# Kernel optimization log

Measured on AMD Instinct MI355X. Metric: run time of the kernel, lower is better.

The kernel has to match this reference:

```python
import jax, jax.numpy as jnp
import numpy as np

INPUT_DIM = 1024
K_DIM = 1024
V_DIM = 1024
HEAD = 16
N = 4096


def setup_inputs() -> dict:
    key = jax.random.key(0)
    ks = jax.random.split(key, 6)
    # kaiming_uniform_(a=1): bound = sqrt(6 / ((1+1)*fan_in)) = sqrt(3/fan_in)
    def ku(k, shape):
        fan_in = shape[1]
        b = np.sqrt(3.0 / fan_in)
        return jax.random.uniform(k, shape, jnp.float32, -b, b)
    x = jax.random.normal(ks[0], (1, N, INPUT_DIM), jnp.float32)
    Wq = ku(ks[1], (K_DIM, INPUT_DIM))
    Wk = ku(ks[2], (K_DIM, INPUT_DIM))
    Wv = ku(ks[3], (V_DIM, INPUT_DIM))
    Wo = ku(ks[4], (V_DIM, V_DIM))
    bo = jnp.zeros((V_DIM,), jnp.float32)
    return {"x": x, "Wq": Wq, "Wk": Wk, "Wv": Wv, "Wo": Wo, "bo": bo}


def reference(x, Wq, Wk, Wv, Wo, bo):
    # x: [1, N, C]
    n = x.shape[1]
    hd_k = K_DIM // HEAD
    hd_v = V_DIM // HEAD
    q = jnp.einsum('bnc,kc->bnk', x, Wq).reshape(1, n, HEAD, hd_k).transpose(0, 2, 1, 3)
    k = jnp.einsum('bnc,kc->bnk', x, Wk).reshape(1, n, HEAD, hd_k).transpose(0, 2, 1, 3)
    v = jnp.einsum('bnc,kc->bnk', x, Wv).reshape(1, n, HEAD, hd_v).transpose(0, 2, 1, 3)
    scale = 1.0 / np.sqrt(hd_k).astype(np.float32)
    scores = jnp.einsum('bhqd,bhkd->bhqk', q, k) * scale  # [1,H,N,N]
    attn = jax.nn.softmax(scores, axis=-1)
    ctx = jnp.einsum('bhqk,bhkd->bhqd', attn, v)  # [1,H,N,hd_v]
    ctx = ctx.transpose(0, 2, 1, 3).reshape(1, n, V_DIM)
    out = jnp.einsum('bnv,ov->bno', ctx, Wo) + bo
    return out
```

## Files before the change

### kernel.cpp

```cpp
#include <hip/hip_runtime.h>

typedef short bf16x8 __attribute__((ext_vector_type(8)));
typedef float f32x4 __attribute__((ext_vector_type(4)));
typedef float f32x16 __attribute__((ext_vector_type(16)));
typedef unsigned short u16;
typedef unsigned short u16x8 __attribute__((ext_vector_type(8)));
typedef unsigned int u32;
typedef unsigned int u32x2 __attribute__((ext_vector_type(2)));
typedef unsigned int u32x4 __attribute__((ext_vector_type(4)));

#define MFMA16(a, b, c) __builtin_amdgcn_mfma_f32_16x16x32_bf16((a), (b), (c), 0, 0, 0)
#define MFMA32(a, b, c) __builtin_amdgcn_mfma_f32_32x32x16_bf16((a), (b), (c), 0, 0, 0)

__device__ __forceinline__ u16 f2bf(float f) {
  unsigned u = __builtin_bit_cast(unsigned, f);
  return (u16)((u + 0x7fffu + ((u >> 16) & 1u)) >> 16);
}

__device__ __forceinline__ unsigned cvt_pk_bf16(float lo, float hi) {
  unsigned r;
  asm("v_cvt_pk_bf16_f32 %0, %1, %2" : "=v"(r) : "v"(lo), "v"(hi));
  return r;
}

__device__ __forceinline__ void gload_lds16(const u16* g, u16* lds) {
  __builtin_amdgcn_global_load_lds((__attribute__((address_space(1))) void*)g,
                                   (__attribute__((address_space(3))) void*)lds,
                                   16, 0, 0);
}

__device__ __forceinline__ void publish_barrier() {
  asm volatile("s_waitcnt lgkmcnt(0)" ::: "memory");
  __builtin_amdgcn_sched_barrier(0);
  __builtin_amdgcn_s_barrier();
}

__global__ __launch_bounds__(256) void cvt_all(
    const float* __restrict__ x, const float* __restrict__ w0,
    const float* __restrict__ w1, const float* __restrict__ w2,
    const float* __restrict__ w3, u16* __restrict__ xb, u16* __restrict__ wb) {
  long i = (long)(blockIdx.x * 256 + threadIdx.x) * 8;
  const float* src; u16* dst; long off;
  if (i < 4194304) { src = x; dst = xb; off = i; }
  else {
    long k = i - 4194304; int w = (int)(k >> 20); off = k & 1048575;
    src = (w == 0) ? w0 : (w == 1) ? w1 : (w == 2) ? w2 : w3;
    dst = wb + (long)w * 1048576;
  }
  float4 a = *(const float4*)(src + off);
  float4 b = *(const float4*)(src + off + 4);
  u16x8 o;
  o[0] = f2bf(a.x); o[1] = f2bf(a.y); o[2] = f2bf(a.z); o[3] = f2bf(a.w);
  o[4] = f2bf(b.x); o[5] = f2bf(b.y); o[6] = f2bf(b.z); o[7] = f2bf(b.w);
  *(u16x8*)(dst + off) = o;
}

template <int MODE>
__global__ __launch_bounds__(256) void gemm_bt(
    const u16* __restrict__ A, const u16* __restrict__ Bw,
    u16* __restrict__ Co, float* __restrict__ Cf, const float* __restrict__ bias) {
  constexpr int K = 1024;
  __shared__ u16 As[128 * 32];
  __shared__ u16 Bs[128 * 32];
  const int tid = threadIdx.x, w = tid >> 6, l = tid & 63;
  const int lg = l >> 4, lr = l & 15;
  const int mb = blockIdx.x;
  int mat, nb;
  if (MODE == 0) { mat = blockIdx.y >> 3; nb = blockIdx.y & 7; }
  else           { mat = 0;               nb = blockIdx.y;     }
  const u16* __restrict__ Bp = Bw + (long)mat * 1048576;
  const int wr = w >> 1, wc = w & 1;
  f32x4 acc[4][4] = {};
  const int srow = (l >> 2), scol = (l & 3) * 8;
  for (int kt = 0; kt < K / 32; ++kt) {
    const int kb = kt * 32;
    __syncthreads();
#pragma unroll
    for (int i = 0; i < 2; ++i) {
      int r = w * 32 + i * 16 + srow;
      gload_lds16(A  + (long)(mb * 128 + r) * K + kb + scol, &As[(w * 2 + i) * 512]);
      gload_lds16(Bp + (long)(nb * 128 + r) * K + kb + scol, &Bs[(w * 2 + i) * 512]);
    }
    __syncthreads();
    bf16x8 af[4], bf[4];
#pragma unroll
    for (int m = 0; m < 4; ++m) af[m] = *(const bf16x8*)&As[(wr * 64 + m * 16 + lr) * 32 + lg * 8];
#pragma unroll
    for (int n = 0; n < 4; ++n) bf[n] = *(const bf16x8*)&Bs[(wc * 64 + n * 16 + lr) * 32 + lg * 8];
#pragma unroll
    for (int m = 0; m < 4; ++m)
#pragma unroll
      for (int n = 0; n < 4; ++n)
        acc[m][n] = MFMA16(af[m], bf[n], acc[m][n]);
  }
  const int row0 = mb * 128 + wr * 64, col0 = nb * 128 + wc * 64;
#pragma unroll
  for (int m = 0; m < 4; ++m)
#pragma unroll
    for (int n = 0; n < 4; ++n)
#pragma unroll
      for (int rr = 0; rr < 4; ++rr) {
        int row = row0 + m * 16 + lg * 4 + rr;
        int col = col0 + n * 16 + lr;
        float v = acc[m][n][rr];
        if (MODE == 0) {
          if (mat == 0) v *= 0.18033688011112042f;
          Co[(long)mat * 4194304 + (long)row * 1024 + col] = f2bf(v);
        } else {
          Cf[(long)row * 1024 + col] = v + bias[col];
        }
      }
}

__global__ __launch_bounds__(256) void attn(
    const u16* __restrict__ Qg, const u16* __restrict__ Kg,
    const u16* __restrict__ Vg, u16* __restrict__ Og) {
  __shared__ u16 Ksb[2 * 4096];
  __shared__ u16 Vsb[2 * 64 * 72];
  const int tid = threadIdx.x, w = tid >> 6, l = tid & 63;
  const int l31 = l & 31, hi = l >> 5;

  const int lin = blockIdx.x;
  const int xcd = lin & 7, idx = lin >> 3;
  const int head = xcd * 2 + (idx >> 5), qt = idx & 31;
  const int hb = head * 64;
  const int q0 = qt * 128 + w * 32;

  const u16* __restrict__ Kh = Kg + hb;

  bf16x8 qf[4];
#pragma unroll
  for (int st = 0; st < 4; ++st)
    qf[st] = *(const bf16x8*)&Qg[(long)(q0 + l31) * 1024 + hb + st * 16 + hi * 8];

  f32x16 o0 = {}, o1 = {};
  f32x4 lsv = {};

  const int kr = tid >> 3, c8 = tid & 7;
  const u16* Vgp = Vg + hb + c8 * 8;
  bf16x8 va0, va1;

  const int krow = tid >> 3;
  const int ksrc = (((tid & 7) * 16) ^ ((krow & 7) << 4)) >> 1;
  u16* kdst = Ksb + w * 512;

#define KSTAGE(t_, db_)                                                       \
  {                                                                           \
    gload_lds16(Kh + (long)((t_) * 64 + krow) * 1024 + ksrc,                  \
                kdst + (db_) * 4096);                                         \
    gload_lds16(Kh + (long)((t_) * 64 + 32 + krow) * 1024 + ksrc,             \
                kdst + (db_) * 4096 + 2048);                                  \
  }

#define VLOAD(t_)                                                     \
  {                                                                   \
    long r0_ = (long)(t_) * 64 + kr * 2;                              \
    va0 = *(const bf16x8*)&Vgp[r0_ * 1024];                           \
    va1 = *(const bf16x8*)&Vgp[(r0_ + 1) * 1024];                     \
  }

#define VWRITE(db_)                                                       \
  {                                                                       \
    const int cw = (kr ^ (c8 << 2)) * 2;                                  \
    u16* d_ = Vsb + (db_) * 4608;                                         \
    u32x4 A_ = __builtin_bit_cast(u32x4, va0);                            \
    u32x4 B_ = __builtin_bit_cast(u32x4, va1);                            \
    _Pragma("unroll") for (int dd = 0; dd < 4; ++dd) {                    \
      u32 pe = __builtin_amdgcn_perm(B_[dd], A_[dd], 0x05040100u);        \
      u32 po = __builtin_amdgcn_perm(B_[dd], A_[dd], 0x07060302u);        \
      *(u32*)&d_[(c8 * 8 + 2 * dd) * 72 + cw] = pe;                       \
      *(u32*)&d_[(c8 * 8 + 2 * dd + 1) * 72 + cw] = po;                   \
    }                                                                     \
  }

#define KFRAG(kf_, db_)                                                       \
  {                                                                           \
    _Pragma("unroll") for (int tt = 0; tt < 2; ++tt)                          \
      _Pragma("unroll") for (int st = 0; st < 4; ++st) {                      \
        const int row_ = tt * 32 + l31;                                       \
        const int boff_ = (st * 32 + hi * 16) ^ ((row_ & 7) << 4);            \
        (kf_)[tt][st] =                                                       \
            *(const bf16x8*)&Ksb[(db_) * 4096 + row_ * 64 + (boff_ >> 1)];    \
      }                                                                       \
  }

#define QKT(S0_, S1_, db_)                                                    \
  {                                                                           \
    bf16x8 kf_[2][4];                                                         \
    KFRAG(kf_, db_);                                                          \
    S0_ = (f32x16){};                                                         \
    S1_ = (f32x16){};                                                         \
    __builtin_amdgcn_s_setprio(1);                                            \
    _Pragma("unroll") for (int st = 0; st < 4; ++st) {                        \
      S0_ = MFMA32(kf_[0][st], qf[st], S0_);                                  \
      S1_ = MFMA32(kf_[1][st], qf[st], S1_);                                  \
    }                                                                         \
    __builtin_amdgcn_s_setprio(0);                                            \
  }

#define PACKCHUNK(SX, base_, pb_)                                             \
  {                                                                           \
    u32 a0_ = cvt_pk_bf16((SX)[(base_) + 0], (SX)[(base_) + 1]);              \
    u32 b0_ = cvt_pk_bf16((SX)[(base_) + 4], (SX)[(base_) + 5]);              \
    u32 a1_ = cvt_pk_bf16((SX)[(base_) + 2], (SX)[(base_) + 3]);              \
    u32 b1_ = cvt_pk_bf16((SX)[(base_) + 6], (SX)[(base_) + 7]);              \
    u32x2 r0_ = __builtin_amdgcn_permlane32_swap(a0_, b0_, false, false);     \
    u32x2 r1_ = __builtin_amdgcn_permlane32_swap(a1_, b1_, false, false);     \
    u32x4 fv_;                                                                \
    fv_[0] = r0_[0]; fv_[1] = r1_[0]; fv_[2] = r0_[1]; fv_[3] = r1_[1];       \
    (pb_) = __builtin_bit_cast(bf16x8, fv_);                                  \
  }

#define FINISH(SC0, SC1, db_)                                                 \
  {                                                                           \
    _Pragma("unroll") for (int r = 0; r < 16; ++r) {                          \
      SC0[r] = __builtin_amdgcn_exp2f(SC0[r]);                                \
      SC1[r] = __builtin_amdgcn_exp2f(SC1[r]);                                \
    }                                                                         \
    const u16* myV = Vsb + (db_) * 4608;                                      \
    _Pragma("unroll") for (int c = 0; c < 4; ++c) {                           \
      bf16x8 pb;                                                              \
      if (c < 2) { PACKCHUNK(SC0, (c & 1) * 8, pb); }                         \
      else       { PACKCHUNK(SC1, (c & 1) * 8, pb); }                         \
      const int sw0 = ((8 * c + 4 * hi) ^ (((l31 >> 3) & 7) << 2)) * 2;       \
      const int sw1 = ((8 * c + 4 * hi) ^ ((((l31 + 32) >> 3) & 7) << 2)) * 2;\
      bf16x8 vf0 = *(const bf16x8*)&myV[l31 * 72 + sw0];                      \
      bf16x8 vf1 = *(const bf16x8*)&myV[(32 + l31) * 72 + sw1];               \
      __builtin_amdgcn_s_setprio(1);                                          \
      o0 = MFMA32(vf0, pb, o0);                                               \
      o1 = MFMA32(vf1, pb, o1);                                               \
      __builtin_amdgcn_s_setprio(0);                                          \
    }                                                                         \
    _Pragma("unroll") for (int r2 = 0; r2 < 4; ++r2)                          \
      _Pragma("unroll") for (int j = 0; j < 4; ++j)                           \
        lsv[j] += SC0[r2 * 4 + j] + SC1[r2 * 4 + j];                          \
  }

  f32x16 Sa0, Sa1, Sb0, Sb1;

  KSTAGE(0, 0);
  VLOAD(0);
  asm volatile("s_waitcnt vmcnt(0)" ::: "memory");
  publish_barrier();
  QKT(Sa0, Sa1, 0);
  KSTAGE(1, 1);
  VWRITE(0);
  asm volatile("s_waitcnt vmcnt(0)" ::: "memory");
  publish_barrier();

#define BODY(t_, db_, SC0, SC1, SN0, SN1)                                     \
  {                                                                           \
    KSTAGE((t_) + 2, db_);                                                    \
    VLOAD((t_) + 1);                                                          \
    QKT(SN0, SN1, (db_) ^ 1);                                                 \
    FINISH(SC0, SC1, db_);                                                    \
    VWRITE((db_) ^ 1);                                                        \
    publish_barrier();                                                        \
  }

  for (int i = 0; i < 31; ++i) {
    BODY(2 * i, 0, Sa0, Sa1, Sb0, Sb1);
    BODY(2 * i + 1, 1, Sb0, Sb1, Sa0, Sa1);
  }
  {
    VLOAD(63);
    QKT(Sb0, Sb1, 1);
    FINISH(Sa0, Sa1, 0);
    VWRITE(1);
    publish_barrier();
  }
  FINISH(Sb0, Sb1, 1);

  {
    float sls = (lsv[0] + lsv[1]) + (lsv[2] + lsv[3]);
    float s = sls + __shfl_xor(sls, 32);
    float inv = 1.0f / s;
#pragma unroll
    for (int dt = 0; dt < 2; ++dt) {
#pragma unroll
      for (int r2 = 0; r2 < 4; ++r2) {
        float v0 = dt ? o1[r2 * 4 + 0] : o0[r2 * 4 + 0];
        float v1 = dt ? o1[r2 * 4 + 1] : o0[r2 * 4 + 1];
        float v2 = dt ? o1[r2 * 4 + 2] : o0[r2 * 4 + 2];
        float v3 = dt ? o1[r2 * 4 + 3] : o0[r2 * 4 + 3];
        uint2 pk;
        pk.x = cvt_pk_bf16(v0 * inv, v1 * inv);
        pk.y = cvt_pk_bf16(v2 * inv, v3 * inv);
        const int d0 = dt * 32 + 8 * r2 + 4 * hi;
        *(uint2*)&Og[(long)(q0 + l31) * 1024 + hb + d0] = pk;
      }
    }
  }
#undef KSTAGE
#undef VLOAD
#undef VWRITE
#undef KFRAG
#undef QKT
#undef PACKCHUNK
#undef FINISH
#undef BODY
}

extern "C" void kernel_launch(void* const* d_in, const int* in_sizes, int n_in,
                              void* d_out, int out_size, void* d_ws, size_t ws_size,
                              hipStream_t stream) {
  const float* x  = (const float*)d_in[0];
  const float* Wq = (const float*)d_in[1];
  const float* Wk = (const float*)d_in[2];
  const float* Wv = (const float*)d_in[3];
  const float* Wo = (const float*)d_in[4];
  const float* bo = (const float*)d_in[5];
  float* out = (float*)d_out;

  u16* xb  = (u16*)d_ws;
  u16* wb  = xb + 4194304;
  u16* qkv = wb + 4194304;
  u16* ctx = qkv + 3 * 4194304;

  cvt_all<<<dim3(4096), dim3(256), 0, stream>>>(x, Wq, Wk, Wv, Wo, xb, wb);
  gemm_bt<0><<<dim3(32, 24), dim3(256), 0, stream>>>(xb, wb, qkv, nullptr, nullptr);
  attn<<<dim3(512), dim3(256), 0, stream>>>(qkv, qkv + 4194304, qkv + 8388608, ctx);
  gemm_bt<1><<<dim3(32, 8), dim3(256), 0, stream>>>(ctx, wb + 3 * 1048576, nullptr, out, bo);
}
```

Baseline: 161.1 us.

## Process two KV tiles per barrier interval with quad-buffered K/V LDS

Restructures the attention main loop so each barrier interval stages and consumes two 64-key tiles, using four LDS buffers for K and V instead of two. Barrier count is halved and the next pair of tiles is prefetched while the current pair runs QK^T and PV. In exchange, LDS use doubles (to about 68KB per block), which may lower occupancy. The skewed pipeline that overlapped the next tile's QK^T with the current tile's softmax/PV is dropped, and more registers are live for the extra V loads and score tiles.

```diff
diff --git a/kernel.cpp b/kernel.cpp
--- a/kernel.cpp
+++ b/kernel.cpp
@@ -115,8 +115,8 @@
 __global__ __launch_bounds__(256) void attn(
     const u16* __restrict__ Qg, const u16* __restrict__ Kg,
     const u16* __restrict__ Vg, u16* __restrict__ Og) {
-  __shared__ u16 Ksb[2 * 4096];
-  __shared__ u16 Vsb[2 * 64 * 72];
+  __shared__ u16 Ksb[4 * 4096];
+  __shared__ u16 Vsb[4 * 4608];
   const int tid = threadIdx.x, w = tid >> 6, l = tid & 63;
   const int l31 = l & 31, hi = l >> 5;
 
@@ -138,39 +138,52 @@
 
   const int kr = tid >> 3, c8 = tid & 7;
   const u16* Vgp = Vg + hb + c8 * 8;
-  bf16x8 va0, va1;
+  bf16x8 va0, va1, vb0, vb1;
 
   const int krow = tid >> 3;
   const int ksrc = (((tid & 7) * 16) ^ ((krow & 7) << 4)) >> 1;
   u16* kdst = Ksb + w * 512;
 
-#define KSTAGE(t_, db_)                                                       \
+#define KSTAGE2(t_, b0_, b1_)                                                 \
   {                                                                           \
     gload_lds16(Kh + (long)((t_) * 64 + krow) * 1024 + ksrc,                  \
-                kdst + (db_) * 4096);                                         \
+                kdst + (b0_) * 4096);                                         \
     gload_lds16(Kh + (long)((t_) * 64 + 32 + krow) * 1024 + ksrc,             \
-                kdst + (db_) * 4096 + 2048);                                  \
-  }
-
-#define VLOAD(t_)                                                     \
+                kdst + (b0_) * 4096 + 2048);                                  \
+    gload_lds16(Kh + (long)((t_) * 64 + 64 + krow) * 1024 + ksrc,             \
+                kdst + (b1_) * 4096);                                         \
+    gload_lds16(Kh + (long)((t_) * 64 + 96 + krow) * 1024 + ksrc,             \
+                kdst + (b1_) * 4096 + 2048);                                  \
+  }
+
+#define VLOAD2(t_)                                                    \
   {                                                                   \
     long r0_ = (long)(t_) * 64 + kr * 2;                              \
     va0 = *(const bf16x8*)&Vgp[r0_ * 1024];                           \
     va1 = *(const bf16x8*)&Vgp[(r0_ + 1) * 1024];                     \
-  }
-
-#define VWRITE(db_)                                                       \
-  {                                                                       \
-    const int cw = (kr ^ (c8 << 2)) * 2;                                  \
-    u16* d_ = Vsb + (db_) * 4608;                                         \
-    u32x4 A_ = __builtin_bit_cast(u32x4, va0);                            \
-    u32x4 B_ = __builtin_bit_cast(u32x4, va1);                            \
-    _Pragma("unroll") for (int dd = 0; dd < 4; ++dd) {                    \
-      u32 pe = __builtin_amdgcn_perm(B_[dd], A_[dd], 0x05040100u);        \
-      u32 po = __builtin_amdgcn_perm(B_[dd], A_[dd], 0x07060302u);        \
-      *(u32*)&d_[(c8 * 8 + 2 * dd) * 72 + cw] = pe;                       \
-      *(u32*)&d_[(c8 * 8 + 2 * dd + 1) * 72 + cw] = po;                   \
-    }                                                                     \
+    vb0 = *(const bf16x8*)&Vgp[(r0_ + 64) * 1024];                    \
+    vb1 = *(const bf16x8*)&Vgp[(r0_ + 65) * 1024];                    \
+  }
+
+#define VWRITE2(b0_, b1_)                                                  \
+  {                                                                        \
+    const int cw = (kr ^ (c8 << 2)) * 2;                                   \
+    u16* da_ = Vsb + (b0_) * 4608;                                         \
+    u16* db_ = Vsb + (b1_) * 4608;                                         \
+    u32x4 A_ = __builtin_bit_cast(u32x4, va0);                             \
+    u32x4 B_ = __builtin_bit_cast(u32x4, va1);                             \
+    u32x4 C_ = __builtin_bit_cast(u32x4, vb0);                             \
+    u32x4 D_ = __builtin_bit_cast(u32x4, vb1);                             \
+    _Pragma("unroll") for (int dd = 0; dd < 4; ++dd) {                     \
+      u32 pe = __builtin_amdgcn_perm(B_[dd], A_[dd], 0x05040100u);         \
+      u32 po = __builtin_amdgcn_perm(B_[dd], A_[dd], 0x07060302u);         \
+      u32 qe = __builtin_amdgcn_perm(D_[dd], C_[dd], 0x05040100u);         \
+      u32 qo = __builtin_amdgcn_perm(D_[dd], C_[dd], 0x07060302u);         \
+      *(u32*)&da_[(c8 * 8 + 2 * dd) * 72 + cw] = pe;                       \
+      *(u32*)&da_[(c8 * 8 + 2 * dd + 1) * 72 + cw] = po;                   \
+      *(u32*)&db_[(c8 * 8 + 2 * dd) * 72 + cw] = qe;                       \
+      *(u32*)&db_[(c8 * 8 + 2 * dd + 1) * 72 + cw] = qo;                   \
+    }                                                                      \
   }
 
 #define KFRAG(kf_, db_)                                                       \
@@ -236,40 +249,33 @@
         lsv[j] += SC0[r2 * 4 + j] + SC1[r2 * 4 + j];                          \
   }
 
-  f32x16 Sa0, Sa1, Sb0, Sb1;
-
-  KSTAGE(0, 0);
-  VLOAD(0);
+#define INTERVAL(i_, p_, stage_)                                              \
+  {                                                                           \
+    if (stage_) {                                                             \
+      KSTAGE2(2 * (i_) + 2, (p_) ^ 2, ((p_) ^ 2) + 1);                        \
+      VLOAD2(2 * (i_) + 2);                                                   \
+    }                                                                         \
+    f32x16 Sa0, Sa1, Sb0, Sb1;                                                \
+    QKT(Sa0, Sa1, p_);                                                        \
+    QKT(Sb0, Sb1, (p_) + 1);                                                  \
+    FINISH(Sa0, Sa1, p_);                                                     \
+    FINISH(Sb0, Sb1, (p_) + 1);                                               \
+    if (stage_) VWRITE2((p_) ^ 2, ((p_) ^ 2) + 1);                            \
+    publish_barrier();                                                        \
+  }
+
+  KSTAGE2(0, 0, 1);
+  VLOAD2(0);
+  VWRITE2(0, 1);
   asm volatile("s_waitcnt vmcnt(0)" ::: "memory");
   publish_barrier();
-  QKT(Sa0, Sa1, 0);
-  KSTAGE(1, 1);
-  VWRITE(0);
-  asm volatile("s_waitcnt vmcnt(0)" ::: "memory");
-  publish_barrier();
-
-#define BODY(t_, db_, SC0, SC1, SN0, SN1)                                     \
-  {                                                                           \
-    KSTAGE((t_) + 2, db_);                                                    \
-    VLOAD((t_) + 1);                                                          \
-    QKT(SN0, SN1, (db_) ^ 1);                                                 \
-    FINISH(SC0, SC1, db_);                                                    \
-    VWRITE((db_) ^ 1);                                                        \
-    publish_barrier();                                                        \
-  }
-
-  for (int i = 0; i < 31; ++i) {
-    BODY(2 * i, 0, Sa0, Sa1, Sb0, Sb1);
-    BODY(2 * i + 1, 1, Sb0, Sb1, Sa0, Sa1);
-  }
-  {
-    VLOAD(63);
-    QKT(Sb0, Sb1, 1);
-    FINISH(Sa0, Sa1, 0);
-    VWRITE(1);
-    publish_barrier();
-  }
-  FINISH(Sb0, Sb1, 1);
+
+  for (int j = 0; j < 15; ++j) {
+    INTERVAL(2 * j, 0, true);
+    INTERVAL(2 * j + 1, 2, true);
+  }
+  INTERVAL(30, 0, true);
+  INTERVAL(31, 2, false);
 
   {
     float sls = (lsv[0] + lsv[1]) + (lsv[2] + lsv[3]);
@@ -291,14 +297,14 @@
       }
     }
   }
-#undef KSTAGE
-#undef VLOAD
-#undef VWRITE
+#undef KSTAGE2
+#undef VLOAD2
+#undef VWRITE2
 #undef KFRAG
 #undef QKT
 #undef PACKCHUNK
 #undef FINISH
-#undef BODY
+#undef INTERVAL
 }
 
 extern "C" void kernel_launch(void* const* d_in, const int* in_sizes, int n_in,
```

Measured after the change: 178.2 us. +10.6%, slower.

## Stage V via direct global-to-LDS loads and transpose-read with ds_read_b64_tr_b16

Applied to the files above, without the earlier changes.

Replaces the register round-trip for V (global load into VGPRs, byte permutes, scattered LDS stores) with direct global-to-LDS async loads, then reads V fragments transposed through ds_read_b64_tr_b16. The aim is to cut VALU permute work, LDS store traffic and register pressure in the attention main loop. It adds a full lgkmcnt wait plus a sched_barrier before the PV MFMAs, and a vmcnt(0) wait every iteration, which may expose load latency. It also depends on the padded LDS layout matching what the transpose-read instruction expects.

```diff
diff --git a/kernel.cpp b/kernel.cpp
--- a/kernel.cpp
+++ b/kernel.cpp
@@ -116,7 +116,7 @@
     const u16* __restrict__ Qg, const u16* __restrict__ Kg,
     const u16* __restrict__ Vg, u16* __restrict__ Og) {
   __shared__ u16 Ksb[2 * 4096];
-  __shared__ u16 Vsb[2 * 64 * 72];
+  __shared__ u16 Vst[2 * 4160];
   const int tid = threadIdx.x, w = tid >> 6, l = tid & 63;
   const int l31 = l & 31, hi = l >> 5;
 
@@ -136,10 +136,6 @@
   f32x16 o0 = {}, o1 = {};
   f32x4 lsv = {};
 
-  const int kr = tid >> 3, c8 = tid & 7;
-  const u16* Vgp = Vg + hb + c8 * 8;
-  bf16x8 va0, va1;
-
   const int krow = tid >> 3;
   const int ksrc = (((tid & 7) * 16) ^ ((krow & 7) << 4)) >> 1;
   u16* kdst = Ksb + w * 512;
@@ -150,27 +146,6 @@
                 kdst + (db_) * 4096);                                         \
     gload_lds16(Kh + (long)((t_) * 64 + 32 + krow) * 1024 + ksrc,             \
                 kdst + (db_) * 4096 + 2048);                                  \
-  }
-
-#define VLOAD(t_)                                                     \
-  {                                                                   \
-    long r0_ = (long)(t_) * 64 + kr * 2;                              \
-    va0 = *(const bf16x8*)&Vgp[r0_ * 1024];                           \
-    va1 = *(const bf16x8*)&Vgp[(r0_ + 1) * 1024];                     \
-  }
-
-#define VWRITE(db_)                                                       \
-  {                                                                       \
-    const int cw = (kr ^ (c8 << 2)) * 2;                                  \
-    u16* d_ = Vsb + (db_) * 4608;                                         \
-    u32x4 A_ = __builtin_bit_cast(u32x4, va0);                            \
-    u32x4 B_ = __builtin_bit_cast(u32x4, va1);                            \
-    _Pragma("unroll") for (int dd = 0; dd < 4; ++dd) {                    \
-      u32 pe = __builtin_amdgcn_perm(B_[dd], A_[dd], 0x05040100u);        \
-      u32 po = __builtin_amdgcn_perm(B_[dd], A_[dd], 0x07060302u);        \
-      *(u32*)&d_[(c8 * 8 + 2 * dd) * 72 + cw] = pe;                       \
-      *(u32*)&d_[(c8 * 8 + 2 * dd + 1) * 72 + cw] = po;                   \
-    }                                                                     \
   }
 
 #define KFRAG(kf_, db_)                                                       \
@@ -211,26 +186,68 @@
     (pb_) = __builtin_bit_cast(bf16x8, fv_);                                  \
   }
 
-#define FINISH(SC0, SC1, db_)                                                 \
+  const int vsk = (w & 1) * 32 + (l >> 1);
+  const int vsd0 = (w >> 1) * 16 + (l & 1) * 8;
+  const int vdbase = (w >> 1) * 1040 + (w & 1) * 512;
+
+#define VSTAGE_TR(t_, db_)                                                    \
+  {                                                                           \
+    gload_lds16(Vg + (long)((t_) * 64 + vsk) * 1024 + hb + vsd0,              \
+                Vst + (db_) * 4160 + vdbase);                                 \
+    gload_lds16(Vg + (long)((t_) * 64 + vsk) * 1024 + hb + vsd0 + 32,         \
+                Vst + (db_) * 4160 + vdbase + 2080);                          \
+  }
+
+  const u32 vtr_base =
+      (u32)(unsigned long long)(void*)Vst +
+      (u32)((l31 >> 4) * 2080 + (l & 15) * 8 + hi * 256);
+
+#define TRREAD(r_, va_, IMM)                                                  \
+  asm volatile("ds_read_b64_tr_b16 %0, %1 offset:" #IMM                       \
+               : "=v"(r_) : "v"(va_));
+
+#define FINISH_TR(SC0, SC1, db_)                                              \
   {                                                                           \
     _Pragma("unroll") for (int r = 0; r < 16; ++r) {                          \
       SC0[r] = __builtin_amdgcn_exp2f(SC0[r]);                                \
       SC1[r] = __builtin_amdgcn_exp2f(SC1[r]);                                \
     }                                                                         \
-    const u16* myV = Vsb + (db_) * 4608;                                      \
-    _Pragma("unroll") for (int c = 0; c < 4; ++c) {                           \
-      bf16x8 pb;                                                              \
-      if (c < 2) { PACKCHUNK(SC0, (c & 1) * 8, pb); }                         \
-      else       { PACKCHUNK(SC1, (c & 1) * 8, pb); }                         \
-      const int sw0 = ((8 * c + 4 * hi) ^ (((l31 >> 3) & 7) << 2)) * 2;       \
-      const int sw1 = ((8 * c + 4 * hi) ^ ((((l31 + 32) >> 3) & 7) << 2)) * 2;\
-      bf16x8 vf0 = *(const bf16x8*)&myV[l31 * 72 + sw0];                      \
-      bf16x8 vf1 = *(const bf16x8*)&myV[(32 + l31) * 72 + sw1];               \
-      __builtin_amdgcn_s_setprio(1);                                          \
-      o0 = MFMA32(vf0, pb, o0);                                               \
-      o1 = MFMA32(vf1, pb, o1);                                               \
-      __builtin_amdgcn_s_setprio(0);                                          \
-    }                                                                         \
+    const u32 va_ = vtr_base + (u32)((db_) * 8320);                           \
+    u32x2 t00, t01, t02, t03, t10, t11, t12, t13;                             \
+    u32x2 t20, t21, t22, t23, t30, t31, t32, t33;                             \
+    TRREAD(t00, va_, 0);    TRREAD(t01, va_, 128);                            \
+    TRREAD(t02, va_, 4160); TRREAD(t03, va_, 4288);                           \
+    TRREAD(t10, va_, 512);  TRREAD(t11, va_, 640);                            \
+    TRREAD(t12, va_, 4672); TRREAD(t13, va_, 4800);                           \
+    TRREAD(t20, va_, 1024); TRREAD(t21, va_, 1152);                           \
+    TRREAD(t22, va_, 5184); TRREAD(t23, va_, 5312);                           \
+    TRREAD(t30, va_, 1536); TRREAD(t31, va_, 1664);                           \
+    TRREAD(t32, va_, 5696); TRREAD(t33, va_, 5824);                           \
+    bf16x8 pb0, pb1, pb2, pb3;                                                \
+    PACKCHUNK(SC0, 0, pb0);                                                   \
+    PACKCHUNK(SC0, 8, pb1);                                                   \
+    PACKCHUNK(SC1, 0, pb2);                                                   \
+    PACKCHUNK(SC1, 8, pb3);                                                   \
+    asm volatile("s_waitcnt lgkmcnt(0)" ::: "memory");                        \
+    __builtin_amdgcn_sched_barrier(0);     \
+    __builtin_amdgcn_s_setprio(1);                                            \
+    { u32x4 f_; f_[0]=t00[0]; f_[1]=t00[1]; f_[2]=t01[0]; f_[3]=t01[1];       \
+      o0 = MFMA32(__builtin_bit_cast(bf16x8, f_), pb0, o0); }                 \
+    { u32x4 f_; f_[0]=t02[0]; f_[1]=t02[1]; f_[2]=t03[0]; f_[3]=t03[1];       \
+      o1 = MFMA32(__builtin_bit_cast(bf16x8, f_), pb0, o1); }                 \
+    { u32x4 f_; f_[0]=t10[0]; f_[1]=t10[1]; f_[2]=t11[0]; f_[3]=t11[1];       \
+      o0 = MFMA32(__builtin_bit_cast(bf16x8, f_), pb1, o0); }                 \
+    { u32x4 f_; f_[0]=t12[0]; f_[1]=t12[1]; f_[2]=t13[0]; f_[3]=t13[1];       \
+      o1 = MFMA32(__builtin_bit_cast(bf16x8, f_), pb1, o1); }                 \
+    { u32x4 f_; f_[0]=t20[0]; f_[1]=t20[1]; f_[2]=t21[0]; f_[3]=t21[1];       \
+      o0 = MFMA32(__builtin_bit_cast(bf16x8, f_), pb2, o0); }                 \
+    { u32x4 f_; f_[0]=t22[0]; f_[1]=t22[1]; f_[2]=t23[0]; f_[3]=t23[1];       \
+      o1 = MFMA32(__builtin_bit_cast(bf16x8, f_), pb2, o1); }                 \
+    { u32x4 f_; f_[0]=t30[0]; f_[1]=t30[1]; f_[2]=t31[0]; f_[3]=t31[1];       \
+      o0 = MFMA32(__builtin_bit_cast(bf16x8, f_), pb3, o0); }                 \
+    { u32x4 f_; f_[0]=t32[0]; f_[1]=t32[1]; f_[2]=t33[0]; f_[3]=t33[1];       \
+      o1 = MFMA32(__builtin_bit_cast(bf16x8, f_), pb3, o1); }                 \
+    __builtin_amdgcn_s_setprio(0);                                            \
     _Pragma("unroll") for (int r2 = 0; r2 < 4; ++r2)                          \
       _Pragma("unroll") for (int j = 0; j < 4; ++j)                           \
         lsv[j] += SC0[r2 * 4 + j] + SC1[r2 * 4 + j];                          \
@@ -239,37 +256,30 @@
   f32x16 Sa0, Sa1, Sb0, Sb1;
 
   KSTAGE(0, 0);
-  VLOAD(0);
+  VSTAGE_TR(0, 0);
   asm volatile("s_waitcnt vmcnt(0)" ::: "memory");
   publish_barrier();
   QKT(Sa0, Sa1, 0);
   KSTAGE(1, 1);
-  VWRITE(0);
   asm volatile("s_waitcnt vmcnt(0)" ::: "memory");
   publish_barrier();
 
-#define BODY(t_, db_, SC0, SC1, SN0, SN1)                                     \
-  {                                                                           \
-    KSTAGE((t_) + 2, db_);                                                    \
-    VLOAD((t_) + 1);                                                          \
+#define BODY_TR(t_, db_, SC0, SC1, SN0, SN1, kst_)                            \
+  {                                                                           \
+    if (kst_) KSTAGE((t_) + 2, db_);                                          \
+    VSTAGE_TR((t_) + 1, (db_) ^ 1);                                           \
     QKT(SN0, SN1, (db_) ^ 1);                                                 \
-    FINISH(SC0, SC1, db_);                                                    \
-    VWRITE((db_) ^ 1);                                                        \
+    FINISH_TR(SC0, SC1, db_);                                                 \
+    asm volatile("s_waitcnt vmcnt(0)" ::: "memory");                          \
     publish_barrier();                                                        \
   }
 
   for (int i = 0; i < 31; ++i) {
-    BODY(2 * i, 0, Sa0, Sa1, Sb0, Sb1);
-    BODY(2 * i + 1, 1, Sb0, Sb1, Sa0, Sa1);
-  }
-  {
-    VLOAD(63);
-    QKT(Sb0, Sb1, 1);
-    FINISH(Sa0, Sa1, 0);
-    VWRITE(1);
-    publish_barrier();
-  }
-  FINISH(Sb0, Sb1, 1);
+    BODY_TR(2 * i, 0, Sa0, Sa1, Sb0, Sb1, true);
+    BODY_TR(2 * i + 1, 1, Sb0, Sb1, Sa0, Sa1, true);
+  }
+  BODY_TR(62, 0, Sa0, Sa1, Sb0, Sb1, false);
+  FINISH_TR(Sb0, Sb1, 1);
 
   {
     float sls = (lsv[0] + lsv[1]) + (lsv[2] + lsv[3]);
@@ -292,13 +302,13 @@
     }
   }
 #undef KSTAGE
-#undef VLOAD
-#undef VWRITE
 #undef KFRAG
 #undef QKT
 #undef PACKCHUNK
-#undef FINISH
-#undef BODY
+#undef VSTAGE_TR
+#undef TRREAD
+#undef FINISH_TR
+#undef BODY_TR
 }
 
 extern "C" void kernel_launch(void* const* d_in, const int* in_sizes, int n_in,
```

Result: no change. 159.0 us (-1.3%).
